# Optimization experiments

Hardware: AMD Instinct MI355X
Metric: run time of the kernel (lower is better)

The kernel has to match this reference:

```python
import jax, jax.numpy as jnp
import numpy as np

H = 20          # hidden_size
IN = 2          # GRU input / l1 output dim


def setup_inputs() -> dict:
    key = jax.random.key(0)
    ks = jax.random.split(key, 7)
    B = 32768
    s = 1.0 / np.sqrt(H)  # torch default init scale
    hidden = jax.random.normal(ks[0], (1, B, H), dtype=jnp.float32)
    w_ih = jax.random.uniform(ks[1], (3 * H, IN), jnp.float32, -s, s)
    w_hh = jax.random.uniform(ks[2], (3 * H, H), jnp.float32, -s, s)
    b_ih = jax.random.uniform(ks[3], (3 * H,), jnp.float32, -s, s)
    b_hh = jax.random.uniform(ks[4], (3 * H,), jnp.float32, -s, s)
    w_l = jax.random.uniform(ks[5], (IN, H), jnp.float32, -s, s)
    b_l = jax.random.uniform(ks[6], (IN,), jnp.float32, -s, s)
    return {"hidden": hidden, "w_ih": w_ih, "w_hh": w_hh,
            "b_ih": b_ih, "b_hh": b_hh, "w_l": w_l, "b_l": b_l,
            "step": 200}


def reference(hidden, w_ih, w_hh, b_ih, b_hh, w_l, b_l, step):
    reverse = True
    B = hidden.shape[1]
    h0 = hidden[0]                      # [B, H]
    x0 = jnp.zeros((B, IN), hidden.dtype)  # first GRU input is zeros

    def gru_step(carry, _):
        h, x = carry
        gi = x @ w_ih.T + b_ih          # [B, 3H]
        gh = h @ w_hh.T + b_hh          # [B, 3H]
        ir, iz, inn = jnp.split(gi, 3, axis=-1)
        hr, hz, hn = jnp.split(gh, 3, axis=-1)
        r = jax.nn.sigmoid(ir + hr)
        z = jax.nn.sigmoid(iz + hz)
        n = jnp.tanh(inn + r * hn)
        h_new = (1.0 - z) * n + z * h   # [B, H]
        y = h_new @ w_l.T + b_l         # [B, 2] -> next input
        return (h_new, y), y

    (_, _), ys = jax.lax.scan(gru_step, (h0, x0), None, length=step)
    # ys: [step, B, 2]; original appends per-step then reverses the list
    if reverse:
        ys = ys[::-1]
    return jnp.transpose(ys, (1, 0, 2))  # [B, step, 2]
```

## Files before the change

### kernel.cpp

```cpp
#include <hip/hip_runtime.h>

#define HDIM 20
#define BLOCK 256

typedef __fp16 half8 __attribute__((ext_vector_type(8)));
typedef __fp16 half2v __attribute__((ext_vector_type(2)));
typedef float  float4v __attribute__((ext_vector_type(4)));
typedef int    int4v  __attribute__((ext_vector_type(4)));

static __device__ __forceinline__ float4v mfma16(half8 a, half8 b, float4v c) {
    return __builtin_amdgcn_mfma_f32_16x16x32_f16(a, b, c, 0, 0, 0);
}


__global__ __launch_bounds__(BLOCK, 2) void gru_decoder_kernel(
    const float* __restrict__ hidden,
    const float* __restrict__ w_ih,
    const float* __restrict__ w_hh,
    const float* __restrict__ b_ih,
    const float* __restrict__ b_hh,
    const float* __restrict__ w_l,
    const float* __restrict__ b_l,
    const int*  __restrict__ step_ptr,
    float* __restrict__ out,
    int B)
{
    const int tid = threadIdx.x;
    const int l   = tid & 63;
    const int wv  = tid >> 6;
    const int el  = l & 15;
    const int q   = l >> 4;
    const int e   = (blockIdx.x * 4 + wv) * 16 + el;
    const int step = *step_ptr;

    const float NL2E  = -1.4426950408889634f;
    const float T2L2E =  2.8853900817779268f;

    const int u_dst = el >> 2;
    const int g     = el & 3;

    half8 Afold[5], Azero[5], Ay;
    #pragma unroll
    for (int T = 0; T < 5; ++T) {
        const int u  = 4 * T + u_dst;
        const int rr = (g == 0) ? u : (g == 1) ? 20 + u : 40 + u;
        const float sc = (g <= 1) ? NL2E : T2L2E;
        half8 hf, h0;
        #pragma unroll
        for (int j = 0; j < 8; ++j) {
            float af = 0.f, a0 = 0.f;
            if (j < 5) {
                const int uk = 4 * j + q;
                float wx = w_ih[rr * 2 + 0] * w_l[uk] + w_ih[rr * 2 + 1] * w_l[HDIM + uk];
                float wh = w_hh[rr * HDIM + uk];
                if (g <= 1)      { af = wh + wx; a0 = wh; }
                else if (g == 2) { af = wx;      a0 = 0.f; }
                else             { af = wh;      a0 = wh; }
            } else if (j == 7 && q == 0) {
                float bx = w_ih[rr * 2 + 0] * b_l[0] + w_ih[rr * 2 + 1] * b_l[1];
                if (g <= 1)      { af = b_ih[rr] + b_hh[rr] + bx; a0 = b_ih[rr] + b_hh[rr]; }
                else if (g == 2) { af = b_ih[rr] + bx;            a0 = b_ih[rr]; }
                else             { af = b_hh[rr];                 a0 = b_hh[rr]; }
            }
            hf[j] = (__fp16)(af * sc);
            h0[j] = (__fp16)(a0 * sc);
        }
        Afold[T] = hf;
        Azero[T] = h0;
    }
    {
        half8 hy;
        #pragma unroll
        for (int j = 0; j < 8; ++j) {
            float v = 0.f;
            if (el < 2) {
                if (j < 5)                 v = w_l[el * HDIM + 4 * j + q];
                else if (j == 7 && q == 0) v = b_l[el];
            }
            hy[j] = (__fp16)v;
        }
        Ay = hy;
    }

    int w3const;
    {
        half2v c67; c67[0] = (__fp16)0.f; c67[1] = (__fp16)((q == 0) ? 1.f : 0.f);
        w3const = __builtin_bit_cast(int, c67);
    }

    float hprev[5];
    half8 Bf;
    {
        const float* hb = hidden + (size_t)e * HDIM;
        #pragma unroll
        for (int T = 0; T < 5; ++T) hprev[T] = hb[4 * T + q];
        int4v bi;
        bi[0] = __builtin_bit_cast(int, __builtin_amdgcn_cvt_pkrtz(hprev[0], hprev[1]));
        bi[1] = __builtin_bit_cast(int, __builtin_amdgcn_cvt_pkrtz(hprev[2], hprev[3]));
        bi[2] = __builtin_bit_cast(int, __builtin_amdgcn_cvt_pkrtz(hprev[4], 0.f));
        bi[3] = w3const;
        Bf = __builtin_bit_cast(half8, bi);
    }

    const float4v czero = {0.f, 0.f, 0.f, 0.f};

    auto do_step = [&](const half8* A) {
        float4v C[5];
        #pragma unroll
        for (int T = 0; T < 5; ++T) C[T] = mfma16(A[T], Bf, czero);
        #pragma unroll
        for (int T = 0; T < 5; ++T) {
            float r = __builtin_amdgcn_rcpf(1.f + __builtin_amdgcn_exp2f(C[T][0]));
            float z = __builtin_amdgcn_rcpf(1.f + __builtin_amdgcn_exp2f(C[T][1]));
            float npre2 = __builtin_fmaf(r, C[T][3], C[T][2]);
            float tn = __builtin_amdgcn_rcpf(1.f + __builtin_amdgcn_exp2f(npre2));
            float n = __builtin_fmaf(-2.f, tn, 1.f);
            hprev[T] = __builtin_fmaf(z, hprev[T] - n, n);
        }
        int4v bi;
        bi[0] = __builtin_bit_cast(int, __builtin_amdgcn_cvt_pkrtz(hprev[0], hprev[1]));
        bi[1] = __builtin_bit_cast(int, __builtin_amdgcn_cvt_pkrtz(hprev[2], hprev[3]));
        bi[2] = __builtin_bit_cast(int, __builtin_amdgcn_cvt_pkrtz(hprev[4], 0.f));
        bi[3] = w3const;
        Bf = __builtin_bit_cast(half8, bi);
    };

    float* outp = out + (size_t)e * 2 * step;

    do_step(Azero);
    for (int t = 1; t < step; ++t) {
        float4v cy = mfma16(Ay, Bf, czero);
        if (q == 0) {
            float2 st; st.x = cy[0]; st.y = cy[1];
            *(float2*)(outp + 2 * (step - t)) = st;
        }
        do_step(Afold);
    }
    {
        float4v cy = mfma16(Ay, Bf, czero);
        if (q == 0) {
            float2 st; st.x = cy[0]; st.y = cy[1];
            *(float2*)(outp + 0) = st;
        }
    }
}

extern "C" void kernel_launch(void* const* d_in, const int* in_sizes, int n_in,
                              void* d_out, int out_size, void* d_ws, size_t ws_size,
                              hipStream_t stream) {
    const float* hidden = (const float*)d_in[0];
    const float* w_ih   = (const float*)d_in[1];
    const float* w_hh   = (const float*)d_in[2];
    const float* b_ih   = (const float*)d_in[3];
    const float* b_hh   = (const float*)d_in[4];
    const float* w_l    = (const float*)d_in[5];
    const float* b_l    = (const float*)d_in[6];
    const int*   step   = (const int*)d_in[7];
    float* out = (float*)d_out;

    int B = in_sizes[0] / HDIM;
    int grid = B / 64;

    gru_decoder_kernel<<<grid, BLOCK, 0, stream>>>(
        hidden, w_ih, w_hh, b_ih, b_hh, w_l, b_l, step, out, B);
}
```

Before: 168.6 us.

## Process two 16-sample batch tiles per wave with packed float2 gate math

Each 64-thread block now holds one wave that handles two independent 16-element batch tiles, interleaving their MFMAs and gate computations. The elementwise update is written with two-element float vectors so the compiler can emit packed FP32 ops. The goal is to raise instruction-level parallelism in the latency-bound sequential recurrence by overlapping two independent dependency chains in one wave. In exchange there are half as many waves overall (1024 instead of 2048) and more registers per wave, which lowers the latency hiding available across waves.

```diff
diff --git a/kernel.cpp b/kernel.cpp
--- a/kernel.cpp
+++ b/kernel.cpp
@@ -1,11 +1,12 @@
 #include <hip/hip_runtime.h>
 
 #define HDIM 20
-#define BLOCK 256
+#define BLOCK 64
 
 typedef __fp16 half8 __attribute__((ext_vector_type(8)));
 typedef __fp16 half2v __attribute__((ext_vector_type(2)));
 typedef float  float4v __attribute__((ext_vector_type(4)));
+typedef float  float2v __attribute__((ext_vector_type(2)));
 typedef int    int4v  __attribute__((ext_vector_type(4)));
 
 static __device__ __forceinline__ float4v mfma16(half8 a, half8 b, float4v c) {
@@ -13,7 +14,7 @@
 }
 
 
-__global__ __launch_bounds__(BLOCK, 2) void gru_decoder_kernel(
+__global__ __launch_bounds__(BLOCK, 1) void gru_decoder_kernel(
     const float* __restrict__ hidden,
     const float* __restrict__ w_ih,
     const float* __restrict__ w_hh,
@@ -25,12 +26,11 @@
     float* __restrict__ out,
     int B)
 {
-    const int tid = threadIdx.x;
-    const int l   = tid & 63;
-    const int wv  = tid >> 6;
+    const int l   = threadIdx.x & 63;
     const int el  = l & 15;
     const int q   = l >> 4;
-    const int e   = (blockIdx.x * 4 + wv) * 16 + el;
+    const int eA  = blockIdx.x * 32 + el;
+    const int eB  = eA + 16;
     const int step = *step_ptr;
 
     const float NL2E  = -1.4426950408889634f;
@@ -88,59 +88,97 @@
         w3const = __builtin_bit_cast(int, c67);
     }
 
-    float hprev[5];
-    half8 Bf;
-    {
-        const float* hb = hidden + (size_t)e * HDIM;
-        #pragma unroll
-        for (int T = 0; T < 5; ++T) hprev[T] = hb[4 * T + q];
-        int4v bi;
-        bi[0] = __builtin_bit_cast(int, __builtin_amdgcn_cvt_pkrtz(hprev[0], hprev[1]));
-        bi[1] = __builtin_bit_cast(int, __builtin_amdgcn_cvt_pkrtz(hprev[2], hprev[3]));
-        bi[2] = __builtin_bit_cast(int, __builtin_amdgcn_cvt_pkrtz(hprev[4], 0.f));
-        bi[3] = w3const;
-        Bf = __builtin_bit_cast(half8, bi);
+    float2v hp[5];
+    half8 BfA, BfB;
+    {
+        const float* ha = hidden + (size_t)eA * HDIM;
+        const float* hb = hidden + (size_t)eB * HDIM;
+        #pragma unroll
+        for (int T = 0; T < 5; ++T) {
+            hp[T][0] = ha[4 * T + q];
+            hp[T][1] = hb[4 * T + q];
+        }
+        int4v ba, bb;
+        ba[0] = __builtin_bit_cast(int, __builtin_amdgcn_cvt_pkrtz(hp[0][0], hp[1][0]));
+        ba[1] = __builtin_bit_cast(int, __builtin_amdgcn_cvt_pkrtz(hp[2][0], hp[3][0]));
+        ba[2] = __builtin_bit_cast(int, __builtin_amdgcn_cvt_pkrtz(hp[4][0], 0.f));
+        ba[3] = w3const;
+        bb[0] = __builtin_bit_cast(int, __builtin_amdgcn_cvt_pkrtz(hp[0][1], hp[1][1]));
+        bb[1] = __builtin_bit_cast(int, __builtin_amdgcn_cvt_pkrtz(hp[2][1], hp[3][1]));
+        bb[2] = __builtin_bit_cast(int, __builtin_amdgcn_cvt_pkrtz(hp[4][1], 0.f));
+        bb[3] = w3const;
+        BfA = __builtin_bit_cast(half8, ba);
+        BfB = __builtin_bit_cast(half8, bb);
     }
 
     const float4v czero = {0.f, 0.f, 0.f, 0.f};
 
     auto do_step = [&](const half8* A) {
-        float4v C[5];
-        #pragma unroll
-        for (int T = 0; T < 5; ++T) C[T] = mfma16(A[T], Bf, czero);
+        float4v CA[5], CB[5];
         #pragma unroll
         for (int T = 0; T < 5; ++T) {
-            float r = __builtin_amdgcn_rcpf(1.f + __builtin_amdgcn_exp2f(C[T][0]));
-            float z = __builtin_amdgcn_rcpf(1.f + __builtin_amdgcn_exp2f(C[T][1]));
-            float npre2 = __builtin_fmaf(r, C[T][3], C[T][2]);
-            float tn = __builtin_amdgcn_rcpf(1.f + __builtin_amdgcn_exp2f(npre2));
-            float n = __builtin_fmaf(-2.f, tn, 1.f);
-            hprev[T] = __builtin_fmaf(z, hprev[T] - n, n);
-        }
-        int4v bi;
-        bi[0] = __builtin_bit_cast(int, __builtin_amdgcn_cvt_pkrtz(hprev[0], hprev[1]));
-        bi[1] = __builtin_bit_cast(int, __builtin_amdgcn_cvt_pkrtz(hprev[2], hprev[3]));
-        bi[2] = __builtin_bit_cast(int, __builtin_amdgcn_cvt_pkrtz(hprev[4], 0.f));
-        bi[3] = w3const;
-        Bf = __builtin_bit_cast(half8, bi);
+            CA[T] = mfma16(A[T], BfA, czero);
+            CB[T] = mfma16(A[T], BfB, czero);
+        }
+        #pragma unroll
+        for (int T = 0; T < 5; ++T) {
+            float2v c0; c0[0] = CA[T][0]; c0[1] = CB[T][0];
+            float2v c1; c1[0] = CA[T][1]; c1[1] = CB[T][1];
+            float2v c2; c2[0] = CA[T][2]; c2[1] = CB[T][2];
+            float2v c3; c3[0] = CA[T][3]; c3[1] = CB[T][3];
+            float2v e0, e1;
+            e0[0] = __builtin_amdgcn_exp2f(c0[0]); e0[1] = __builtin_amdgcn_exp2f(c0[1]);
+            e1[0] = __builtin_amdgcn_exp2f(c1[0]); e1[1] = __builtin_amdgcn_exp2f(c1[1]);
+            float2v a0 = e0 + 1.f;
+            float2v a1 = e1 + 1.f;
+            float2v r, z;
+            r[0] = __builtin_amdgcn_rcpf(a0[0]); r[1] = __builtin_amdgcn_rcpf(a0[1]);
+            z[0] = __builtin_amdgcn_rcpf(a1[0]); z[1] = __builtin_amdgcn_rcpf(a1[1]);
+            float2v np = c2 + r * c3;
+            float2v e2;
+            e2[0] = __builtin_amdgcn_exp2f(np[0]); e2[1] = __builtin_amdgcn_exp2f(np[1]);
+            float2v a2 = e2 + 1.f;
+            float2v tn;
+            tn[0] = __builtin_amdgcn_rcpf(a2[0]); tn[1] = __builtin_amdgcn_rcpf(a2[1]);
+            float2v n = 1.f - 2.f * tn;
+            hp[T] = n + z * (hp[T] - n);
+        }
+        int4v ba, bb;
+        ba[0] = __builtin_bit_cast(int, __builtin_amdgcn_cvt_pkrtz(hp[0][0], hp[1][0]));
+        ba[1] = __builtin_bit_cast(int, __builtin_amdgcn_cvt_pkrtz(hp[2][0], hp[3][0]));
+        ba[2] = __builtin_bit_cast(int, __builtin_amdgcn_cvt_pkrtz(hp[4][0], 0.f));
+        ba[3] = w3const;
+        bb[0] = __builtin_bit_cast(int, __builtin_amdgcn_cvt_pkrtz(hp[0][1], hp[1][1]));
+        bb[1] = __builtin_bit_cast(int, __builtin_amdgcn_cvt_pkrtz(hp[2][1], hp[3][1]));
+        bb[2] = __builtin_bit_cast(int, __builtin_amdgcn_cvt_pkrtz(hp[4][1], 0.f));
+        bb[3] = w3const;
+        BfA = __builtin_bit_cast(half8, ba);
+        BfB = __builtin_bit_cast(half8, bb);
     };
 
-    float* outp = out + (size_t)e * 2 * step;
+    float* outA = out + (size_t)eA * 2 * step;
+    float* outB = out + (size_t)eB * 2 * step;
 
     do_step(Azero);
     for (int t = 1; t < step; ++t) {
-        float4v cy = mfma16(Ay, Bf, czero);
+        float4v cyA = mfma16(Ay, BfA, czero);
+        float4v cyB = mfma16(Ay, BfB, czero);
         if (q == 0) {
-            float2 st; st.x = cy[0]; st.y = cy[1];
-            *(float2*)(outp + 2 * (step - t)) = st;
+            float2 sa; sa.x = cyA[0]; sa.y = cyA[1];
+            float2 sb; sb.x = cyB[0]; sb.y = cyB[1];
+            *(float2*)(outA + 2 * (step - t)) = sa;
+            *(float2*)(outB + 2 * (step - t)) = sb;
         }
         do_step(Afold);
     }
     {
-        float4v cy = mfma16(Ay, Bf, czero);
+        float4v cyA = mfma16(Ay, BfA, czero);
+        float4v cyB = mfma16(Ay, BfB, czero);
         if (q == 0) {
-            float2 st; st.x = cy[0]; st.y = cy[1];
-            *(float2*)(outp + 0) = st;
+            float2 sa; sa.x = cyA[0]; sa.y = cyA[1];
+            float2 sb; sb.x = cyB[0]; sb.y = cyB[1];
+            *(float2*)(outA + 0) = sa;
+            *(float2*)(outB + 0) = sb;
         }
     }
 }
@@ -159,7 +197,7 @@
     float* out = (float*)d_out;
 
     int B = in_sizes[0] / HDIM;
-    int grid = B / 64;
+    int grid = B / 32;
 
     gru_decoder_kernel<<<grid, BLOCK, 0, stream>>>(
         hidden, w_ih, w_hh, b_ih, b_hh, w_l, b_l, step, out, B);
```

Result: slower. 175.9 us (+4.3%).

## Replace sigmoid/tanh transcendentals with shared-memory piecewise-linear lookup table

Applied to the files above, without the earlier changes.

Builds a 512-entry fp16 sigmoid table with slopes in LDS at kernel start, and evaluates the reset gate and the tanh candidate by linear interpolation instead of exp2+rcp. Weight scaling factors are changed so the MFMA outputs land directly in table index units. This cuts transcendental-unit work per step in exchange for LDS reads and reduced accuracy from table resolution and clamping.

```diff
diff --git a/kernel.cpp b/kernel.cpp
--- a/kernel.cpp
+++ b/kernel.cpp
@@ -25,7 +25,20 @@
     float* __restrict__ out,
     int B)
 {
+    __shared__ unsigned tab[512];
+
     const int tid = threadIdx.x;
+    const float L2E = 1.4426950408889634f;
+    for (int i = tid; i < 512; i += BLOCK) {
+        float x0 = (float)(i - 256) * (1.0f / 32.0f);
+        float x1 = x0 + 1.0f / 32.0f;
+        float y0 = 1.0f / (1.0f + __builtin_amdgcn_exp2f(-x0 * L2E));
+        float y1 = 1.0f / (1.0f + __builtin_amdgcn_exp2f(-x1 * L2E));
+        half2v bs; bs[0] = (__fp16)y0; bs[1] = (__fp16)(y1 - y0);
+        tab[i] = __builtin_bit_cast(unsigned, bs);
+    }
+    __syncthreads();
+
     const int l   = tid & 63;
     const int wv  = tid >> 6;
     const int el  = l & 15;
@@ -33,8 +46,9 @@
     const int e   = (blockIdx.x * 4 + wv) * 16 + el;
     const int step = *step_ptr;
 
-    const float NL2E  = -1.4426950408889634f;
-    const float T2L2E =  2.8853900817779268f;
+    const float NL2E = -1.4426950408889634f;
+    const float SR   = 32.0f;
+    const float SN   = 64.0f;
 
     const int u_dst = el >> 2;
     const int g     = el & 3;
@@ -44,7 +58,7 @@
     for (int T = 0; T < 5; ++T) {
         const int u  = 4 * T + u_dst;
         const int rr = (g == 0) ? u : (g == 1) ? 20 + u : 40 + u;
-        const float sc = (g <= 1) ? NL2E : T2L2E;
+        const float sc = (g == 0) ? SR : (g == 1) ? NL2E : SN;
         half8 hf, h0;
         #pragma unroll
         for (int j = 0; j < 8; ++j) {
@@ -104,17 +118,27 @@
 
     const float4v czero = {0.f, 0.f, 0.f, 0.f};
 
+    auto lut = [&](float t) -> float {
+        float u = t + 256.f;
+        u = __builtin_amdgcn_fmed3f(u, 0.f, 511.9995f);
+        int i = (int)u;
+        float f = __builtin_amdgcn_fractf(u);
+        half2v bs = __builtin_bit_cast(half2v, tab[i]);
+        return __builtin_fmaf(f, (float)bs[1], (float)bs[0]);
+    };
+
     auto do_step = [&](const half8* A) {
         float4v C[5];
         #pragma unroll
         for (int T = 0; T < 5; ++T) C[T] = mfma16(A[T], Bf, czero);
         #pragma unroll
         for (int T = 0; T < 5; ++T) {
-            float r = __builtin_amdgcn_rcpf(1.f + __builtin_amdgcn_exp2f(C[T][0]));
-            float z = __builtin_amdgcn_rcpf(1.f + __builtin_amdgcn_exp2f(C[T][1]));
-            float npre2 = __builtin_fmaf(r, C[T][3], C[T][2]);
-            float tn = __builtin_amdgcn_rcpf(1.f + __builtin_amdgcn_exp2f(npre2));
-            float n = __builtin_fmaf(-2.f, tn, 1.f);
+            float r = lut(C[T][0]);
+            float ez = __builtin_amdgcn_exp2f(C[T][1]);
+            float z = __builtin_amdgcn_rcpf(1.f + ez);
+            float tn = __builtin_fmaf(r, C[T][3], C[T][2]);
+            float sn = lut(tn);
+            float n = __builtin_fmaf(2.f, sn, -1.f);
             hprev[T] = __builtin_fmaf(z, hprev[T] - n, n);
         }
         int4v bi;
```

Result: slower. 190.4 us (+12.9%).
